# Kernel tuning notes

Hardware: AMD Instinct MI355X
Metric: run time of the kernel (lower is better)

## Reference

```python
import jax, jax.numpy as jnp
import numpy as np

N_VARS = 1024      # code length n
N_CHECKS = 512     # number of parity checks m
VAR_DEG = 3        # column degree -> E = N_VARS * VAR_DEG edges
N_EDGES = N_VARS * VAR_DEG
BATCH = 2048
CLIP_TANH = 10.0
ENSEMBLE_NUM = 3


def _make_edges():
    # Regular LDPC-like Tanner graph: each variable node connects to VAR_DEG distinct checks.
    rng = np.random.default_rng(0)
    edge_var = np.repeat(np.arange(N_VARS, dtype=np.int32), VAR_DEG)
    edge_chk = np.concatenate([
        rng.choice(N_CHECKS, size=VAR_DEG, replace=False).astype(np.int32)
        for _ in range(N_VARS)
    ])
    return jnp.asarray(edge_var), jnp.asarray(edge_chk)


def setup_inputs() -> dict:
    key = jax.random.key(0)
    k1, k2, k3, k4, k5 = jax.random.split(key, 5)
    edge_var, edge_chk = _make_edges()
    return {
        "x": jax.random.normal(k1, (BATCH, N_EDGES), dtype=jnp.float32),
        "llr": jax.random.normal(k2, (BATCH, N_VARS), dtype=jnp.float32),
        "odd_weights": jax.random.normal(k3, (N_EDGES, N_EDGES), dtype=jnp.float32) * 0.05,
        "llr_weights": jax.random.normal(k4, (N_VARS, N_EDGES), dtype=jnp.float32) * 0.05,
        "dropout_logits": jnp.full((N_EDGES,), 3.0, dtype=jnp.float32),  # LOGITS_INIT
        "edge_var": edge_var,
        "edge_chk": edge_chk,
    }


def reference(x, llr, odd_weights, llr_weights, dropout_logits, edge_var, edge_chk):
    dt = x.dtype
    # Tanner-graph masks (constant connectivity)
    # w_skipconn2even_mask: [n, E], 1 where edge e is incident to variable v
    w_skip_mask = (jnp.arange(N_VARS)[:, None] == edge_var[None, :]).astype(dt)
    # w_odd2even_mask: [E, E], 1 where edges share a variable but differ in check (extrinsic)
    w_odd_mask = ((edge_var[:, None] == edge_var[None, :]) &
                  (edge_chk[:, None] != edge_chk[None, :])).astype(dt)

    x_after_mask = x @ (w_odd_mask * odd_weights)                 # [B, E]
    odd_weights_times_llr = llr @ (w_skip_mask * llr_weights)     # [B, E]

    keep_prob = jax.nn.sigmoid(dropout_logits)                    # [E]
    keys = jax.random.split(jax.random.key(42), ENSEMBLE_NUM)

    def member(k):
        u = jax.random.uniform(k, odd_weights_times_llr.shape, dtype=dt)
        z = (u < keep_prob).astype(dt)                            # dropout_ori
        odd = jnp.clip(x_after_mask + odd_weights_times_llr * z,
                       -CLIP_TANH, CLIP_TANH)
        return jnp.tanh(0.5 * odd)

    return jnp.mean(jax.vmap(member)(keys), axis=0)              # ensemble average
```

## Files before the change

### kernel.cpp

```cpp
#include <hip/hip_runtime.h>
#include <stdint.h>
#include <cmath>

#define NVARS   1024
#define NEDGES  3072
#define BATCHSZ 2048
#define HALF_B  (BATCHSZ/2)
#define CLIPT   10.0f

#define PARTITIONABLE 1

__host__ __device__ __forceinline__ void tf_round(uint32_t& x0, uint32_t& x1, int r) {
    x0 += x1;
    x1 = (x1 << r) | (x1 >> (32 - r));
    x1 ^= x0;
}

__host__ __device__ __forceinline__ void threefry2x32(uint32_t k0, uint32_t k1,
                                                      uint32_t x0, uint32_t x1,
                                                      uint32_t& o0, uint32_t& o1) {
    uint32_t k2 = k0 ^ k1 ^ 0x1BD11BDAu;
    x0 += k0; x1 += k1;
    tf_round(x0, x1, 13); tf_round(x0, x1, 15); tf_round(x0, x1, 26); tf_round(x0, x1, 6);
    x0 += k1; x1 += k2 + 1u;
    tf_round(x0, x1, 17); tf_round(x0, x1, 29); tf_round(x0, x1, 16); tf_round(x0, x1, 24);
    x0 += k2; x1 += k0 + 2u;
    tf_round(x0, x1, 13); tf_round(x0, x1, 15); tf_round(x0, x1, 26); tf_round(x0, x1, 6);
    x0 += k0; x1 += k1 + 3u;
    tf_round(x0, x1, 17); tf_round(x0, x1, 29); tf_round(x0, x1, 16); tf_round(x0, x1, 24);
    x0 += k1; x1 += k2 + 4u;
    tf_round(x0, x1, 13); tf_round(x0, x1, 15); tf_round(x0, x1, 26); tf_round(x0, x1, 6);
    x0 += k2; x1 += k0 + 5u;
    o0 = x0; o1 = x1;
}

__device__ __forceinline__ float tanh_half(float o) {
    float ex = __expf(o);
    return 1.0f - 2.0f * __builtin_amdgcn_rcpf(ex + 1.0f);
}

__global__ void setup_kernel(const float* __restrict__ oddw,
                             const float* __restrict__ llrw,
                             const float* __restrict__ logits,
                             const int* __restrict__ evar,
                             const int* __restrict__ echk,
                             float4* __restrict__ wkp,
                             int4* __restrict__ sidx) {
    int e = blockIdx.x * blockDim.x + threadIdx.x;
    if (e >= NEDGES) return;
    int v = evar[e];
    int r = e % 3;
    int base = e - r;
    int o1 = base + ((r + 1) % 3);
    int o2 = base + ((r + 2) % 3);
    int ce = echk[e];
    float w1 = (echk[o1] != ce) ? oddw[(size_t)o1 * NEDGES + e] : 0.0f;
    float w2 = (echk[o2] != ce) ? oddw[(size_t)o2 * NEDGES + e] : 0.0f;
    float vw = llrw[(size_t)v * NEDGES + e];
    float kp = (float)(1.0 / (1.0 + exp(-(double)logits[e])));
    wkp[e]  = make_float4(w1, w2, vw, kp);
    sidx[e] = make_int4(o1, o2, v, 0);
}

__global__ __launch_bounds__(256) void
odd_layer_kernel(const float* __restrict__ x, const float* __restrict__ llr,
                 const float4* __restrict__ wkp, const int4* __restrict__ sidx,
                 float* __restrict__ out,
                 uint32_t k0a, uint32_t k1a, uint32_t k0b, uint32_t k1b,
                 uint32_t k0c, uint32_t k1c) {
    int e = blockIdx.x * 256 + threadIdx.x;
    int b = blockIdx.y;

    float4 w = wkp[e];
    int4  s = sidx[e];

    const float* xr1 = x + (size_t)b * NEDGES;
    const float* xr2 = xr1 + (size_t)HALF_B * NEDGES;
    float xa1 = xr1[s.x] * w.x + xr1[s.y] * w.y;
    float xa2 = xr2[s.x] * w.x + xr2[s.y] * w.y;
    float t1  = llr[(size_t)b * NVARS + s.z] * w.z;
    float t2  = llr[(size_t)(b + HALF_B) * NVARS + s.z] * w.z;

    uint32_t i1 = (uint32_t)b * NEDGES + (uint32_t)e;
    uint32_t i2 = i1 + (uint32_t)HALF_B * NEDGES;

    const uint32_t K0[3] = {k0a, k0b, k0c};
    const uint32_t K1[3] = {k1a, k1b, k1c};

    float acc1 = 0.0f, acc2 = 0.0f;
#pragma unroll
    for (int j = 0; j < 3; j++) {
        uint32_t bits1, bits2;
#if PARTITIONABLE
        uint32_t a0, a1, b0, b1;
        threefry2x32(K0[j], K1[j], 0u, i1, a0, a1);
        threefry2x32(K0[j], K1[j], 0u, i2, b0, b1);
        bits1 = a0 ^ a1;
        bits2 = b0 ^ b1;
#else
        threefry2x32(K0[j], K1[j], i1, i2, bits1, bits2);
#endif
        float u1 = __uint_as_float((bits1 >> 9) | 0x3f800000u) - 1.0f;
        float u2 = __uint_as_float((bits2 >> 9) | 0x3f800000u) - 1.0f;
        float odd1 = xa1 + ((u1 < w.w) ? t1 : 0.0f);
        float odd2 = xa2 + ((u2 < w.w) ? t2 : 0.0f);
        odd1 = fminf(fmaxf(odd1, -CLIPT), CLIPT);
        odd2 = fminf(fmaxf(odd2, -CLIPT), CLIPT);
        acc1 += tanh_half(odd1);
        acc2 += tanh_half(odd2);
    }
    out[i1] = acc1 * (1.0f / 3.0f);
    out[i2] = acc2 * (1.0f / 3.0f);
}

extern "C" void kernel_launch(void* const* d_in, const int* in_sizes, int n_in,
                              void* d_out, int out_size, void* d_ws, size_t ws_size,
                              hipStream_t stream) {
    const float* x      = (const float*)d_in[0];
    const float* llr    = (const float*)d_in[1];
    const float* oddw   = (const float*)d_in[2];
    const float* llrw   = (const float*)d_in[3];
    const float* logits = (const float*)d_in[4];
    const int*   evar   = (const int*)d_in[5];
    const int*   echk   = (const int*)d_in[6];
    float* out = (float*)d_out;

    float4* wkp  = (float4*)d_ws;
    int4*   sidx = (int4*)((char*)d_ws + (size_t)NEDGES * sizeof(float4));

    uint32_t k0[3], k1[3];
#if PARTITIONABLE
    for (uint32_t j = 0; j < 3; j++) {
        threefry2x32(0u, 42u, 0u, j, k0[j], k1[j]);
    }
#else
    {
        uint32_t o0[3], o1[3];
        for (uint32_t t = 0; t < 3; t++) threefry2x32(0u, 42u, t, t + 3u, o0[t], o1[t]);
        uint32_t outb[6] = {o0[0], o0[1], o0[2], o1[0], o1[1], o1[2]};
        k0[0] = outb[0]; k1[0] = outb[1];
        k0[1] = outb[2]; k1[1] = outb[3];
        k0[2] = outb[4]; k1[2] = outb[5];
    }
#endif

    setup_kernel<<<(NEDGES + 255) / 256, 256, 0, stream>>>(oddw, llrw, logits, evar, echk, wkp, sidx);

    dim3 grid(NEDGES / 256, HALF_B);
    odd_layer_kernel<<<grid, 256, 0, stream>>>(x, llr, wkp, sidx, out,
                                               k0[0], k1[0], k0[1], k1[1], k0[2], k1[2]);
}
```

Before: 47.69 us.

## Count dropout keeps with integer threshold and compute two tanh values per element

The uniform-versus-keep-probability comparison becomes an integer compare against a threshold precomputed in setup, so the float conversion is gone. Each output element now counts how many of the three ensemble members keep the edge and evaluates tanh only for the dropped and kept cases, blending them linearly. This cuts six tanh evaluations per pair of rows down to two per row. Each thread also handles four batch rows instead of two, which halves the grid height and adds register pressure, and the threshold must reproduce the float comparison exactly at rounding edges.

```diff
diff --git a/kernel.cpp b/kernel.cpp
--- a/kernel.cpp
+++ b/kernel.cpp
@@ -5,10 +5,9 @@
 #define NVARS   1024
 #define NEDGES  3072
 #define BATCHSZ 2048
-#define HALF_B  (BATCHSZ/2)
+#define RPT     4
+#define ROWSTR  (BATCHSZ/RPT)
 #define CLIPT   10.0f
-
-#define PARTITIONABLE 1
 
 __host__ __device__ __forceinline__ void tf_round(uint32_t& x0, uint32_t& x1, int r) {
     x0 += x1;
@@ -57,8 +56,12 @@
     float w1 = (echk[o1] != ce) ? oddw[(size_t)o1 * NEDGES + e] : 0.0f;
     float w2 = (echk[o2] != ce) ? oddw[(size_t)o2 * NEDGES + e] : 0.0f;
     float vw = llrw[(size_t)v * NEDGES + e];
-    float kp = (float)(1.0 / (1.0 + exp(-(double)logits[e])));
-    wkp[e]  = make_float4(w1, w2, vw, kp);
+    float kpf = (float)(1.0 / (1.0 + exp(-(double)logits[e])));
+    double Td = ceil((double)kpf * 8388608.0);
+    uint32_t T9;
+    if (Td >= 8388608.0) T9 = 0xFFFFFFFFu;
+    else                 T9 = ((uint32_t)Td) << 9;
+    wkp[e]  = make_float4(w1, w2, vw, __uint_as_float(T9));
     sidx[e] = make_int4(o1, o2, v, 0);
 }
 
@@ -69,48 +72,49 @@
                  uint32_t k0a, uint32_t k1a, uint32_t k0b, uint32_t k1b,
                  uint32_t k0c, uint32_t k1c) {
     int e = blockIdx.x * 256 + threadIdx.x;
-    int b = blockIdx.y;
+    int b0 = blockIdx.y;
 
     float4 w = wkp[e];
-    int4  s = sidx[e];
+    int4   s = sidx[e];
+    uint32_t T9 = __float_as_uint(w.w);
 
-    const float* xr1 = x + (size_t)b * NEDGES;
-    const float* xr2 = xr1 + (size_t)HALF_B * NEDGES;
-    float xa1 = xr1[s.x] * w.x + xr1[s.y] * w.y;
-    float xa2 = xr2[s.x] * w.x + xr2[s.y] * w.y;
-    float t1  = llr[(size_t)b * NVARS + s.z] * w.z;
-    float t2  = llr[(size_t)(b + HALF_B) * NVARS + s.z] * w.z;
-
-    uint32_t i1 = (uint32_t)b * NEDGES + (uint32_t)e;
-    uint32_t i2 = i1 + (uint32_t)HALF_B * NEDGES;
+    float    xa[RPT], tv[RPT];
+    uint32_t idx[RPT];
+    int      cnt[RPT];
+#pragma unroll
+    for (int r = 0; r < RPT; r++) {
+        int b = b0 + r * ROWSTR;
+        const float* xr = x + (size_t)b * NEDGES;
+        float xs1 = xr[s.x];
+        float xs2 = xr[s.y];
+        float lv  = llr[b * NVARS + s.z];
+        xa[r]  = xs1 * w.x + xs2 * w.y;
+        tv[r]  = lv * w.z;
+        idx[r] = (uint32_t)b * NEDGES + (uint32_t)e;
+        cnt[r] = 0;
+    }
 
     const uint32_t K0[3] = {k0a, k0b, k0c};
     const uint32_t K1[3] = {k1a, k1b, k1c};
 
-    float acc1 = 0.0f, acc2 = 0.0f;
 #pragma unroll
     for (int j = 0; j < 3; j++) {
-        uint32_t bits1, bits2;
-#if PARTITIONABLE
-        uint32_t a0, a1, b0, b1;
-        threefry2x32(K0[j], K1[j], 0u, i1, a0, a1);
-        threefry2x32(K0[j], K1[j], 0u, i2, b0, b1);
-        bits1 = a0 ^ a1;
-        bits2 = b0 ^ b1;
-#else
-        threefry2x32(K0[j], K1[j], i1, i2, bits1, bits2);
-#endif
-        float u1 = __uint_as_float((bits1 >> 9) | 0x3f800000u) - 1.0f;
-        float u2 = __uint_as_float((bits2 >> 9) | 0x3f800000u) - 1.0f;
-        float odd1 = xa1 + ((u1 < w.w) ? t1 : 0.0f);
-        float odd2 = xa2 + ((u2 < w.w) ? t2 : 0.0f);
-        odd1 = fminf(fmaxf(odd1, -CLIPT), CLIPT);
-        odd2 = fminf(fmaxf(odd2, -CLIPT), CLIPT);
-        acc1 += tanh_half(odd1);
-        acc2 += tanh_half(odd2);
+#pragma unroll
+        for (int r = 0; r < RPT; r++) {
+            uint32_t o0, o1;
+            threefry2x32(K0[j], K1[j], 0u, idx[r], o0, o1);
+            cnt[r] += ((o0 ^ o1) < T9) ? 1 : 0;
+        }
     }
-    out[i1] = acc1 * (1.0f / 3.0f);
-    out[i2] = acc2 * (1.0f / 3.0f);
+
+#pragma unroll
+    for (int r = 0; r < RPT; r++) {
+        float a0 = fminf(fmaxf(xa[r],          -CLIPT), CLIPT);
+        float a1 = fminf(fmaxf(xa[r] + tv[r],  -CLIPT), CLIPT);
+        float t0 = tanh_half(a0);
+        float t1 = tanh_half(a1);
+        out[idx[r]] = fmaf((float)cnt[r], (t1 - t0) * (1.0f / 3.0f), t0);
+    }
 }
 
 extern "C" void kernel_launch(void* const* d_in, const int* in_sizes, int n_in,
@@ -129,24 +133,13 @@
     int4*   sidx = (int4*)((char*)d_ws + (size_t)NEDGES * sizeof(float4));
 
     uint32_t k0[3], k1[3];
-#if PARTITIONABLE
     for (uint32_t j = 0; j < 3; j++) {
         threefry2x32(0u, 42u, 0u, j, k0[j], k1[j]);
     }
-#else
-    {
-        uint32_t o0[3], o1[3];
-        for (uint32_t t = 0; t < 3; t++) threefry2x32(0u, 42u, t, t + 3u, o0[t], o1[t]);
-        uint32_t outb[6] = {o0[0], o0[1], o0[2], o1[0], o1[1], o1[2]};
-        k0[0] = outb[0]; k1[0] = outb[1];
-        k0[1] = outb[2]; k1[1] = outb[3];
-        k0[2] = outb[4]; k1[2] = outb[5];
-    }
-#endif
 
     setup_kernel<<<(NEDGES + 255) / 256, 256, 0, stream>>>(oddw, llrw, logits, evar, echk, wkp, sidx);
 
-    dim3 grid(NEDGES / 256, HALF_B);
+    dim3 grid(NEDGES / 256, ROWSTR);
     odd_layer_kernel<<<grid, 256, 0, stream>>>(x, llr, wkp, sidx, out,
                                                k0[0], k1[0], k0[1], k1[1], k0[2], k1[2]);
 }
```

After: 47.31 us. About the same (-0.8%).
